# Kernel tuning notes

Hardware: AMD Instinct MI355X
Metric: run time of the kernel (lower is better)

Reference implementation:

```python
import jax, jax.numpy as jnp
import numpy as np

B, N, D, H = 4, 512, 4, 256


def _linear_params(key, fan_in, fan_out):
    # torch.nn.Linear default init: U(-1/sqrt(fan_in), 1/sqrt(fan_in))
    lim = 1.0 / np.sqrt(fan_in)
    kw, kb = jax.random.split(key)
    W = jax.random.uniform(kw, (fan_in, fan_out), minval=-lim, maxval=lim, dtype=jnp.float32)
    b = jax.random.uniform(kb, (fan_out,), minval=-lim, maxval=lim, dtype=jnp.float32)
    return W, b


def setup_inputs() -> dict:
    key = jax.random.key(0)
    ks = jax.random.split(key, 8)
    x = jax.random.normal(ks[0], (B, N, D), dtype=jnp.float32)
    adj = jax.random.uniform(ks[1], (B, N, N), dtype=jnp.float32)  # soft adjacency in [0,1)
    W_e1, b_e1 = _linear_params(ks[2], 2 * D, H)
    W_e2, b_e2 = _linear_params(ks[3], H, H)
    W_n1, b_n1 = _linear_params(ks[4], H, H)
    W_n2, b_n2 = _linear_params(ks[5], H, H)
    W_o1, b_o1 = _linear_params(ks[6], D + H, H)
    W_o, b_o = _linear_params(ks[7], H, D)
    return {
        "x": x, "adj": adj,
        "W_e1": W_e1, "b_e1": b_e1, "W_e2": W_e2, "b_e2": b_e2,
        "W_n1": W_n1, "b_n1": b_n1, "W_n2": W_n2, "b_n2": b_n2,
        "W_o1": W_o1, "b_o1": b_o1, "W_o": W_o, "b_o": b_o,
    }


def reference(x, adj, W_e1, b_e1, W_e2, b_e2, W_n1, b_n1, W_n2, b_n2, W_o1, b_o1, W_o, b_o):
    b_, n_, d_ = x.shape
    # innode[b,i,j,:] = x[b,j]; outnode[b,i,j,:] = x[b,i]
    innode = jnp.broadcast_to(x[:, None, :, :], (b_, n_, n_, d_))
    outnode = jnp.broadcast_to(x[:, :, None, :], (b_, n_, n_, d_))
    edge_in = jnp.concatenate([innode, outnode], axis=-1)          # [B,N,N,2D]
    node2edge = jax.nn.relu(edge_in @ W_e1 + b_e1)                 # [B,N,N,H]
    edge2edge = jax.nn.relu(node2edge @ W_e2 + b_e2)               # [B,N,N,H]
    # adjacency-masked sum over axis 1 (the i axis)
    agg = jnp.einsum('bij,bijh->bjh', adj, edge2edge)              # [B,N,H]
    out1 = jax.nn.relu(agg @ W_n1 + b_n1)
    out2 = jax.nn.relu(out1 @ W_n2 + b_n2)
    out3 = jnp.concatenate([x, out2], axis=-1)                     # [B,N,D+H]
    out4 = out3 @ W_o1 + b_o1
    out5 = out4 @ W_o + b_o                                        # [B,N,D]
    # CONTINUOUS is False for the classifier variant
    return jax.nn.log_softmax(out5, axis=2)
```

## Files before the change

kernel.cpp:

```cpp
#include <hip/hip_runtime.h>
#include <hip/hip_fp16.h>
#include <math.h>

#define Bq 4
#define Nq 512
#define Dq 4
#define Hq 256

typedef _Float16 f16x8 __attribute__((ext_vector_type(8)));
typedef float f32x4 __attribute__((ext_vector_type(4)));

__device__ __forceinline__ f16x8 hadd_relu(f16x8 u, f16x8 v) {
    f16x8 s = u + v;
    const f16x8 z = (f16x8)(_Float16)0.0f;
    return __builtin_elementwise_max(s, z);
}

__device__ __forceinline__ uint4 cvt8h(const float* p) {
    union { __half h[8]; uint4 u; } r;
#pragma unroll
    for (int i = 0; i < 8; ++i) r.h[i] = __float2half(p[i]);
    return r.u;
}

__global__ __launch_bounds__(256) void prep_all(
    const float* __restrict__ x, const float* __restrict__ We1,
    const float* __restrict__ be1, __half* __restrict__ U, __half* __restrict__ V,
    const float* __restrict__ Wn1, const float* __restrict__ Wn2,
    const float* __restrict__ Wo1, __half* __restrict__ Wt16) {
    const int bid = blockIdx.x;
    const int t = threadIdx.x;
    if (bid < 256) {
        const float w0 = We1[0 * 256 + t], w1 = We1[1 * 256 + t];
        const float w2 = We1[2 * 256 + t], w3 = We1[3 * 256 + t];
        const float w4 = We1[4 * 256 + t], w5 = We1[5 * 256 + t];
        const float w6 = We1[6 * 256 + t], w7 = We1[7 * 256 + t];
        const float bv = be1[t];
#pragma unroll
        for (int r = 0; r < 8; ++r) {
            const int row = bid * 8 + r;
            const float* xp = x + row * Dq;
            const float x0 = xp[0], x1 = xp[1], x2 = xp[2], x3 = xp[3];
            float u = bv;
            u = fmaf(x0, w0, u); u = fmaf(x1, w1, u);
            u = fmaf(x2, w2, u); u = fmaf(x3, w3, u);
            float v = x0 * w4;
            v = fmaf(x1, w5, v); v = fmaf(x2, w6, v); v = fmaf(x3, w7, v);
            U[(size_t)row * Hq + t] = __float2half(u);
            V[(size_t)row * Hq + t] = __float2half(v);
        }
    } else {
        __shared__ float ld[64][65];
        const int tid = bid - 256;
        const int mat = tid >> 4;
        const int tile = tid & 15;
        const int k0 = (tile >> 2) * 64;
        const int n0 = (tile & 3) * 64;
        const float* W = (mat == 0) ? Wn1 : (mat == 1) ? Wn2 : (Wo1 + 4 * 256);
        const int rr = t >> 6;
        const int cc = t & 63;
#pragma unroll
        for (int r = 0; r < 16; ++r) {
            const int row = r * 4 + rr;
            ld[row][cc] = W[(size_t)(k0 + row) * 256 + n0 + cc];
        }
        __syncthreads();
#pragma unroll
        for (int r = 0; r < 16; ++r) {
            const int nrow = r * 4 + rr;
            Wt16[((size_t)mat * 256 + n0 + nrow) * 256 + k0 + cc] =
                __float2half(ld[cc][nrow]);
        }
    }
}

__global__ __launch_bounds__(256, 2) void edge_gemm(
    const __half* __restrict__ U, const __half* __restrict__ V,
    const float* __restrict__ We2, const float* __restrict__ be2,
    const float* __restrict__ adj, float* __restrict__ aggws) {
    __shared__ __align__(16) char smem[59392];
    __half* Wt = (__half*)smem;
    __half* Us = (__half*)(smem + 32768);
    __half* Vs = (__half*)(smem + 40960);
    float* adjs = (float*)(smem + 57344);
    float* red = (float*)(smem + 40960);

    const int bid = blockIdx.x;
    const int hq_ = bid & 3;
    const int jt = (bid >> 2) & 31;
    const int b = bid >> 7;
    const int h_base = hq_ * 64;
    const int j_base = jt * 16;
    const int t = threadIdx.x;
    const int lane = t & 63;
    const int w = t >> 6;
    const int q = lane >> 4;
    const int l15 = lane & 15;

    const __half* Vb = V + (size_t)b * Nq * Hq;
    const float* adjb = adj + (size_t)b * Nq * Nq;

    const int srow = t >> 4;
    const int sc0 = (t & 15) * 2;

    {
        const int n = t & 63;
        const int swz = n & 31;
        for (int kk = (t >> 6); kk < 256; kk += 4) {
            float val = We2[kk * 256 + h_base + n];
            Wt[n * 256 + ((((kk >> 3) ^ swz)) << 3) + (kk & 7)] = __float2half(val);
        }
    }
    {
        const uint4* gp = (const uint4*)(U + (size_t)(b * Nq + j_base + srow) * Hq);
        uint4 v0 = gp[sc0];
        uint4 v1 = gp[sc0 + 1];
        *(uint4*)&Us[srow * 256 + ((sc0 ^ srow) << 3)] = v0;
        *(uint4*)&Us[srow * 256 + (((sc0 + 1) ^ srow) << 3)] = v1;
    }

    float bias[4];
#pragma unroll
    for (int nt = 0; nt < 4; ++nt) bias[nt] = be2[h_base + nt * 16 + l15];

    f32x4 agg[4];
#pragma unroll
    for (int nt = 0; nt < 4; ++nt) agg[nt] = (f32x4){0.f, 0.f, 0.f, 0.f};

    uint4 pva, pvb; float pad_;
    {
        const uint4* gp = (const uint4*)(Vb + (size_t)(0 + srow) * Hq);
        pva = gp[sc0]; pvb = gp[sc0 + 1];
        pad_ = adjb[(size_t)(0 + srow) * Nq + j_base + (t & 15)];
        *(uint4*)&Vs[0 * 4096 + srow * 256 + ((sc0 ^ srow) << 3)] = pva;
        *(uint4*)&Vs[0 * 4096 + srow * 256 + (((sc0 + 1) ^ srow) << 3)] = pvb;
        adjs[0 * 256 + t] = pad_;
    }
    {
        const uint4* gp = (const uint4*)(Vb + (size_t)(16 + srow) * Hq);
        pva = gp[sc0]; pvb = gp[sc0 + 1];
        pad_ = adjb[(size_t)(16 + srow) * Nq + j_base + (t & 15)];
    }
    __syncthreads();

    const f32x4 zero4 = (f32x4){0.f, 0.f, 0.f, 0.f};

    for (int ch = 0; ch < 32; ++ch) {
        const int cur = ch & 1;
        const __half* Vcur = Vs + cur * 4096;
        const float* Acur = adjs + cur * 256;

        f32x4 acc[4][4];
#pragma unroll
        for (int mi = 0; mi < 4; ++mi)
#pragma unroll
            for (int nt = 0; nt < 4; ++nt)
                acc[mi][nt] = (f32x4){bias[nt], bias[nt], bias[nt], bias[nt]};

#pragma unroll
        for (int ks = 0; ks < 8; ++ks) {
            const int c = ks * 4 + q;
            const f16x8 uvec = *(const f16x8*)&Us[l15 * 256 + ((c ^ l15) << 3)];
            f16x8 afrag[4];
#pragma unroll
            for (int mi = 0; mi < 4; ++mi) {
                const int iv = w * 4 + mi;
                const f16x8 vvec = *(const f16x8*)&Vcur[iv * 256 + ((c ^ iv) << 3)];
                afrag[mi] = hadd_relu(uvec, vvec);
            }
            f16x8 bf[4];
#pragma unroll
            for (int nt = 0; nt < 4; ++nt) {
                const int rn = nt * 16 + l15;
                bf[nt] = *(const f16x8*)&Wt[rn * 256 + ((c ^ (rn & 31)) << 3)];
            }
#pragma unroll
            for (int mi = 0; mi < 4; ++mi)
#pragma unroll
                for (int nt = 0; nt < 4; ++nt)
                    acc[mi][nt] = __builtin_amdgcn_mfma_f32_16x16x32_f16(
                        afrag[mi], bf[nt], acc[mi][nt], 0, 0, 0);
        }

#pragma unroll
        for (int mi = 0; mi < 4; ++mi) {
            const int iv = w * 4 + mi;
            const f32x4 av = *(const f32x4*)&Acur[iv * 16 + q * 4];
#pragma unroll
            for (int nt = 0; nt < 4; ++nt) {
                const f32x4 rel = __builtin_elementwise_max(acc[mi][nt], zero4);
                agg[nt] = av * rel + agg[nt];
            }
        }

        if (ch < 31) {
            const int nxt = cur ^ 1;
            *(uint4*)&Vs[nxt * 4096 + srow * 256 + ((sc0 ^ srow) << 3)] = pva;
            *(uint4*)&Vs[nxt * 4096 + srow * 256 + (((sc0 + 1) ^ srow) << 3)] = pvb;
            adjs[nxt * 256 + t] = pad_;
            if (ch < 30) {
                const int i_base = (ch + 2) * 16;
                const uint4* gp = (const uint4*)(Vb + (size_t)(i_base + srow) * Hq);
                pva = gp[sc0]; pvb = gp[sc0 + 1];
                pad_ = adjb[(size_t)(i_base + srow) * Nq + j_base + (t & 15)];
            }
        }
        __syncthreads();
    }

#pragma unroll
    for (int nt = 0; nt < 4; ++nt)
#pragma unroll
        for (int r = 0; r < 4; ++r)
            red[w * 1024 + (q * 4 + r) * 64 + nt * 16 + l15] = agg[nt][r];
    __syncthreads();
    {
        const int j = t >> 4;
        const int h0 = (t & 15) * 4;
        f32x4 s = *(const f32x4*)&red[0 * 1024 + j * 64 + h0];
        s += *(const f32x4*)&red[1 * 1024 + j * 64 + h0];
        s += *(const f32x4*)&red[2 * 1024 + j * 64 + h0];
        s += *(const f32x4*)&red[3 * 1024 + j * 64 + h0];
        *(f32x4*)&aggws[(size_t)(b * Nq + j_base + j) * Hq + h_base + h0] = s;
    }
}

__global__ __launch_bounds__(256) void tail_kernel(
    const float* __restrict__ aggws, const float* __restrict__ x,
    const __half* __restrict__ Wt16,
    const float* __restrict__ bn1, const float* __restrict__ bn2,
    const float* __restrict__ Wo1, const float* __restrict__ bo1,
    const float* __restrict__ Wo, const float* __restrict__ bo,
    float* __restrict__ out) {
    __shared__ __align__(16) __half actA[16 * 256];
    __shared__ __align__(16) __half actB[16 * 256];
    __shared__ float xs[16][4];
    __shared__ float part[4][16][4];
    __shared__ float s5[16][4];
    const int g0 = blockIdx.x * 16;
    const int t = threadIdx.x;
    const int lane = t & 63;
    const int w = t >> 6;
    const int q = lane >> 4;
    const int l15 = lane & 15;
    const int hb = w * 64;

    {
        const int row = t >> 4;
        const int g = (t & 15) * 2;
        const float* src = aggws + (size_t)(g0 + row) * 256;
        *(uint4*)&actA[row * 256 + ((g ^ row) << 3)] = cvt8h(src + g * 8);
        *(uint4*)&actA[row * 256 + (((g + 1) ^ row) << 3)] = cvt8h(src + g * 8 + 8);
    }
    if (t < 64) xs[t >> 2][t & 3] = x[(size_t)(g0 + (t >> 2)) * 4 + (t & 3)];
    __syncthreads();

    f32x4 acc[4];
#pragma unroll
    for (int nt = 0; nt < 4; ++nt) {
        const float bv = bn1[hb + nt * 16 + l15];
        acc[nt] = (f32x4){bv, bv, bv, bv};
    }
#pragma unroll
    for (int ks = 0; ks < 8; ++ks) {
        const int c = ks * 4 + q;
        const f16x8 af = *(const f16x8*)&actA[l15 * 256 + ((c ^ l15) << 3)];
#pragma unroll
        for (int nt = 0; nt < 4; ++nt) {
            const f16x8 bf = *(const f16x8*)&Wt16[(size_t)(hb + nt * 16 + l15) * 256 + c * 8];
            acc[nt] = __builtin_amdgcn_mfma_f32_16x16x32_f16(af, bf, acc[nt], 0, 0, 0);
        }
    }
#pragma unroll
    for (int nt = 0; nt < 4; ++nt) {
        const int n = hb + nt * 16 + l15;
        const int g = n >> 3;
#pragma unroll
        for (int r = 0; r < 4; ++r) {
            const int row = q * 4 + r;
            actB[row * 256 + ((g ^ row) << 3) + (n & 7)] = __float2half(fmaxf(acc[nt][r], 0.f));
        }
    }
    __syncthreads();

#pragma unroll
    for (int nt = 0; nt < 4; ++nt) {
        const float bv = bn2[hb + nt * 16 + l15];
        acc[nt] = (f32x4){bv, bv, bv, bv};
    }
#pragma unroll
    for (int ks = 0; ks < 8; ++ks) {
        const int c = ks * 4 + q;
        const f16x8 af = *(const f16x8*)&actB[l15 * 256 + ((c ^ l15) << 3)];
#pragma unroll
        for (int nt = 0; nt < 4; ++nt) {
            const f16x8 bf = *(const f16x8*)&Wt16[65536 + (size_t)(hb + nt * 16 + l15) * 256 + c * 8];
            acc[nt] = __builtin_amdgcn_mfma_f32_16x16x32_f16(af, bf, acc[nt], 0, 0, 0);
        }
    }
#pragma unroll
    for (int nt = 0; nt < 4; ++nt) {
        const int n = hb + nt * 16 + l15;
        const int g = n >> 3;
#pragma unroll
        for (int r = 0; r < 4; ++r) {
            const int row = q * 4 + r;
            actA[row * 256 + ((g ^ row) << 3) + (n & 7)] = __float2half(fmaxf(acc[nt][r], 0.f));
        }
    }
    __syncthreads();

#pragma unroll
    for (int nt = 0; nt < 4; ++nt) {
        const int n = hb + nt * 16 + l15;
        const float bv = bo1[n];
        const float w0 = Wo1[0 * 256 + n], w1 = Wo1[1 * 256 + n];
        const float w2 = Wo1[2 * 256 + n], w3 = Wo1[3 * 256 + n];
#pragma unroll
        for (int r = 0; r < 4; ++r) {
            const int row = q * 4 + r;
            float v = bv;
            v = fmaf(xs[row][0], w0, v); v = fmaf(xs[row][1], w1, v);
            v = fmaf(xs[row][2], w2, v); v = fmaf(xs[row][3], w3, v);
            acc[nt][r] = v;
        }
    }
#pragma unroll
    for (int ks = 0; ks < 8; ++ks) {
        const int c = ks * 4 + q;
        const f16x8 af = *(const f16x8*)&actA[l15 * 256 + ((c ^ l15) << 3)];
#pragma unroll
        for (int nt = 0; nt < 4; ++nt) {
            const f16x8 bf = *(const f16x8*)&Wt16[2 * 65536 + (size_t)(hb + nt * 16 + l15) * 256 + c * 8];
            acc[nt] = __builtin_amdgcn_mfma_f32_16x16x32_f16(af, bf, acc[nt], 0, 0, 0);
        }
    }

    float p[4][4];
#pragma unroll
    for (int r = 0; r < 4; ++r)
#pragma unroll
        for (int d = 0; d < 4; ++d) p[r][d] = 0.f;
#pragma unroll
    for (int nt = 0; nt < 4; ++nt) {
        const int n = hb + nt * 16 + l15;
        const float4 wv = *(const float4*)&Wo[n * 4];
#pragma unroll
        for (int r = 0; r < 4; ++r) {
            p[r][0] = fmaf(acc[nt][r], wv.x, p[r][0]);
            p[r][1] = fmaf(acc[nt][r], wv.y, p[r][1]);
            p[r][2] = fmaf(acc[nt][r], wv.z, p[r][2]);
            p[r][3] = fmaf(acc[nt][r], wv.w, p[r][3]);
        }
    }
#pragma unroll
    for (int off = 1; off < 16; off <<= 1)
#pragma unroll
        for (int r = 0; r < 4; ++r)
#pragma unroll
            for (int d = 0; d < 4; ++d)
                p[r][d] += __shfl_xor(p[r][d], off);
    if (l15 == 0) {
#pragma unroll
        for (int r = 0; r < 4; ++r)
#pragma unroll
            for (int d = 0; d < 4; ++d) part[w][q * 4 + r][d] = p[r][d];
    }
    __syncthreads();
    if (t < 64) {
        const int row = t >> 2;
        const int d = t & 3;
        s5[row][d] = part[0][row][d] + part[1][row][d] + part[2][row][d]
                   + part[3][row][d] + bo[d];
    }
    __syncthreads();
    if (t < 16) {
        const float v0 = s5[t][0], v1 = s5[t][1], v2 = s5[t][2], v3 = s5[t][3];
        const float m = fmaxf(fmaxf(v0, v1), fmaxf(v2, v3));
        const float s = expf(v0 - m) + expf(v1 - m) + expf(v2 - m) + expf(v3 - m);
        const float lse = m + logf(s);
        float* op = out + (size_t)(g0 + t) * 4;
        op[0] = v0 - lse; op[1] = v1 - lse; op[2] = v2 - lse; op[3] = v3 - lse;
    }
}

extern "C" void kernel_launch(void* const* d_in, const int* in_sizes, int n_in,
                              void* d_out, int out_size, void* d_ws, size_t ws_size,
                              hipStream_t stream) {
    const float* x   = (const float*)d_in[0];
    const float* adj = (const float*)d_in[1];
    const float* We1 = (const float*)d_in[2];
    const float* be1 = (const float*)d_in[3];
    const float* We2 = (const float*)d_in[4];
    const float* be2 = (const float*)d_in[5];
    const float* Wn1 = (const float*)d_in[6];
    const float* bn1 = (const float*)d_in[7];
    const float* Wn2 = (const float*)d_in[8];
    const float* bn2 = (const float*)d_in[9];
    const float* Wo1 = (const float*)d_in[10];
    const float* bo1 = (const float*)d_in[11];
    const float* Wo  = (const float*)d_in[12];
    const float* bo  = (const float*)d_in[13];
    float* out = (float*)d_out;

    __half* U = (__half*)d_ws;
    __half* V = U + (size_t)Bq * Nq * Hq;
    float* aggws = (float*)((char*)d_ws + (size_t)2 * Bq * Nq * Hq * sizeof(__half));
    __half* Wt16 = (__half*)((char*)d_ws + (size_t)4 * 1024 * 1024);

    prep_all<<<304, 256, 0, stream>>>(x, We1, be1, U, V, Wn1, Wn2, Wo1, Wt16);
    edge_gemm<<<512, 256, 0, stream>>>(U, V, We2, be2, adj, aggws);
    tail_kernel<<<128, 256, 0, stream>>>(aggws, x, Wt16, bn1, bn2, Wo1, bo1, Wo, bo, out);
}
```

Baseline: 227.3 us.

## Double edge_gemm block to 512 threads with 32-row i chunks

```diff
diff --git a/kernel.cpp b/kernel.cpp
--- a/kernel.cpp
+++ b/kernel.cpp
@@ -74,15 +74,15 @@
     }
 }
 
-__global__ __launch_bounds__(256, 2) void edge_gemm(
+__global__ __launch_bounds__(512, 4) void edge_gemm(
     const __half* __restrict__ U, const __half* __restrict__ V,
     const float* __restrict__ We2, const float* __restrict__ be2,
     const float* __restrict__ adj, float* __restrict__ aggws) {
-    __shared__ __align__(16) char smem[59392];
+    __shared__ __align__(16) char smem[77824];
     __half* Wt = (__half*)smem;
     __half* Us = (__half*)(smem + 32768);
     __half* Vs = (__half*)(smem + 40960);
-    float* adjs = (float*)(smem + 57344);
+    float* adjs = (float*)(smem + 73728);
     float* red = (float*)(smem + 40960);
 
     const int bid = blockIdx.x;
@@ -106,17 +106,19 @@
     {
         const int n = t & 63;
         const int swz = n & 31;
-        for (int kk = (t >> 6); kk < 256; kk += 4) {
+        for (int kk = (t >> 6); kk < 256; kk += 8) {
             float val = We2[kk * 256 + h_base + n];
             Wt[n * 256 + ((((kk >> 3) ^ swz)) << 3) + (kk & 7)] = __float2half(val);
         }
     }
-    {
-        const uint4* gp = (const uint4*)(U + (size_t)(b * Nq + j_base + srow) * Hq);
-        uint4 v0 = gp[sc0];
-        uint4 v1 = gp[sc0 + 1];
-        *(uint4*)&Us[srow * 256 + ((sc0 ^ srow) << 3)] = v0;
-        *(uint4*)&Us[srow * 256 + (((sc0 + 1) ^ srow) << 3)] = v1;
+    if (t < 256) {
+        const int sr = t >> 4;
+        const int g0 = (t & 15) * 2;
+        const uint4* gp = (const uint4*)(U + (size_t)(b * Nq + j_base + sr) * Hq);
+        uint4 v0 = gp[g0];
+        uint4 v1 = gp[g0 + 1];
+        *(uint4*)&Us[sr * 256 + ((g0 ^ sr) << 3)] = v0;
+        *(uint4*)&Us[sr * 256 + (((g0 + 1) ^ sr) << 3)] = v1;
     }
 
     float bias[4];
@@ -129,26 +131,26 @@
 
     uint4 pva, pvb; float pad_;
     {
-        const uint4* gp = (const uint4*)(Vb + (size_t)(0 + srow) * Hq);
+        const uint4* gp = (const uint4*)(Vb + (size_t)srow * Hq);
         pva = gp[sc0]; pvb = gp[sc0 + 1];
-        pad_ = adjb[(size_t)(0 + srow) * Nq + j_base + (t & 15)];
-        *(uint4*)&Vs[0 * 4096 + srow * 256 + ((sc0 ^ srow) << 3)] = pva;
-        *(uint4*)&Vs[0 * 4096 + srow * 256 + (((sc0 + 1) ^ srow) << 3)] = pvb;
-        adjs[0 * 256 + t] = pad_;
+        pad_ = adjb[(size_t)srow * Nq + j_base + (t & 15)];
+        *(uint4*)&Vs[srow * 256 + ((sc0 ^ srow) << 3)] = pva;
+        *(uint4*)&Vs[srow * 256 + (((sc0 + 1) ^ srow) << 3)] = pvb;
+        adjs[t] = pad_;
     }
     {
-        const uint4* gp = (const uint4*)(Vb + (size_t)(16 + srow) * Hq);
+        const uint4* gp = (const uint4*)(Vb + (size_t)(32 + srow) * Hq);
         pva = gp[sc0]; pvb = gp[sc0 + 1];
-        pad_ = adjb[(size_t)(16 + srow) * Nq + j_base + (t & 15)];
+        pad_ = adjb[(size_t)(32 + srow) * Nq + j_base + (t & 15)];
     }
     __syncthreads();
 
     const f32x4 zero4 = (f32x4){0.f, 0.f, 0.f, 0.f};
 
-    for (int ch = 0; ch < 32; ++ch) {
+    for (int ch = 0; ch < 16; ++ch) {
         const int cur = ch & 1;
-        const __half* Vcur = Vs + cur * 4096;
-        const float* Acur = adjs + cur * 256;
+        const __half* Vcur = Vs + cur * 8192;
+        const float* Acur = adjs + cur * 512;
 
         f32x4 acc[4][4];
 #pragma unroll
@@ -193,13 +195,13 @@
             }
         }
 
-        if (ch < 31) {
+        if (ch < 15) {
             const int nxt = cur ^ 1;
-            *(uint4*)&Vs[nxt * 4096 + srow * 256 + ((sc0 ^ srow) << 3)] = pva;
-            *(uint4*)&Vs[nxt * 4096 + srow * 256 + (((sc0 + 1) ^ srow) << 3)] = pvb;
-            adjs[nxt * 256 + t] = pad_;
-            if (ch < 30) {
-                const int i_base = (ch + 2) * 16;
+            *(uint4*)&Vs[nxt * 8192 + srow * 256 + ((sc0 ^ srow) << 3)] = pva;
+            *(uint4*)&Vs[nxt * 8192 + srow * 256 + (((sc0 + 1) ^ srow) << 3)] = pvb;
+            adjs[nxt * 512 + t] = pad_;
+            if (ch < 14) {
+                const int i_base = (ch + 2) * 32;
                 const uint4* gp = (const uint4*)(Vb + (size_t)(i_base + srow) * Hq);
                 pva = gp[sc0]; pvb = gp[sc0 + 1];
                 pad_ = adjb[(size_t)(i_base + srow) * Nq + j_base + (t & 15)];
@@ -214,13 +216,13 @@
         for (int r = 0; r < 4; ++r)
             red[w * 1024 + (q * 4 + r) * 64 + nt * 16 + l15] = agg[nt][r];
     __syncthreads();
-    {
+    if (t < 256) {
         const int j = t >> 4;
         const int h0 = (t & 15) * 4;
         f32x4 s = *(const f32x4*)&red[0 * 1024 + j * 64 + h0];
-        s += *(const f32x4*)&red[1 * 1024 + j * 64 + h0];
-        s += *(const f32x4*)&red[2 * 1024 + j * 64 + h0];
-        s += *(const f32x4*)&red[3 * 1024 + j * 64 + h0];
+#pragma unroll
+        for (int ww = 1; ww < 8; ++ww)
+            s += *(const f32x4*)&red[ww * 1024 + j * 64 + h0];
         *(f32x4*)&aggws[(size_t)(b * Nq + j_base + j) * Hq + h_base + h0] = s;
     }
 }
@@ -409,6 +411,6 @@
     __half* Wt16 = (__half*)((char*)d_ws + (size_t)4 * 1024 * 1024);
 
     prep_all<<<304, 256, 0, stream>>>(x, We1, be1, U, V, Wn1, Wn2, Wo1, Wt16);
-    edge_gemm<<<512, 256, 0, stream>>>(U, V, We2, be2, adj, aggws);
+    edge_gemm<<<512, 512, 0, stream>>>(U, V, We2, be2, adj, aggws);
     tail_kernel<<<128, 256, 0, stream>>>(aggws, x, Wt16, bn1, bn2, Wo1, bo1, Wo, bo, out);
 }
```

Measured after the change: 464.4 us. 104% more time.

## Split edge GEMM over i halves with atomic reduction and global pre-transposed We2

Applied to the files above, without the earlier changes.

```diff
diff --git a/kernel.cpp b/kernel.cpp
--- a/kernel.cpp
+++ b/kernel.cpp
@@ -27,10 +27,17 @@
     const float* __restrict__ x, const float* __restrict__ We1,
     const float* __restrict__ be1, __half* __restrict__ U, __half* __restrict__ V,
     const float* __restrict__ Wn1, const float* __restrict__ Wn2,
-    const float* __restrict__ Wo1, __half* __restrict__ Wt16) {
+    const float* __restrict__ Wo1, const float* __restrict__ We2,
+    __half* __restrict__ Wt16, float* __restrict__ aggz) {
     const int bid = blockIdx.x;
     const int t = threadIdx.x;
     if (bid < 256) {
+        {
+            float* az = aggz + (size_t)bid * 2048 + t * 8;
+            const f32x4 z4 = (f32x4){0.f, 0.f, 0.f, 0.f};
+            *(f32x4*)az = z4;
+            *(f32x4*)(az + 4) = z4;
+        }
         const float w0 = We1[0 * 256 + t], w1 = We1[1 * 256 + t];
         const float w2 = We1[2 * 256 + t], w3 = We1[3 * 256 + t];
         const float w4 = We1[4 * 256 + t], w5 = We1[5 * 256 + t];
@@ -56,7 +63,8 @@
         const int tile = tid & 15;
         const int k0 = (tile >> 2) * 64;
         const int n0 = (tile & 3) * 64;
-        const float* W = (mat == 0) ? Wn1 : (mat == 1) ? Wn2 : (Wo1 + 4 * 256);
+        const float* W = (mat == 0) ? Wn1 : (mat == 1) ? Wn2
+                       : (mat == 2) ? (Wo1 + 4 * 256) : We2;
         const int rr = t >> 6;
         const int cc = t & 63;
 #pragma unroll
@@ -74,23 +82,24 @@
     }
 }
 
-__global__ __launch_bounds__(256, 2) void edge_gemm(
+__global__ __launch_bounds__(256, 4) void edge_gemm(
     const __half* __restrict__ U, const __half* __restrict__ V,
-    const float* __restrict__ We2, const float* __restrict__ be2,
+    const __half* __restrict__ We2t, const float* __restrict__ be2,
     const float* __restrict__ adj, float* __restrict__ aggws) {
-    __shared__ __align__(16) char smem[59392];
-    __half* Wt = (__half*)smem;
-    __half* Us = (__half*)(smem + 32768);
-    __half* Vs = (__half*)(smem + 40960);
-    float* adjs = (float*)(smem + 57344);
-    float* red = (float*)(smem + 40960);
+    __shared__ __align__(16) char smem[26624];
+    __half* Us = (__half*)smem;
+    __half* Vs = (__half*)(smem + 8192);
+    float* adjs = (float*)(smem + 24576);
+    float* red = (float*)(smem + 8192);
 
     const int bid = blockIdx.x;
-    const int hq_ = bid & 3;
-    const int jt = (bid >> 2) & 31;
-    const int b = bid >> 7;
+    const int jt = bid & 31;
+    const int ih = (bid >> 5) & 1;
+    const int hq_ = (bid >> 6) & 3;
+    const int b = bid >> 8;
     const int h_base = hq_ * 64;
     const int j_base = jt * 16;
+    const int i0 = ih * 256;
     const int t = threadIdx.x;
     const int lane = t & 63;
     const int w = t >> 6;
@@ -103,14 +112,6 @@
     const int srow = t >> 4;
     const int sc0 = (t & 15) * 2;
 
-    {
-        const int n = t & 63;
-        const int swz = n & 31;
-        for (int kk = (t >> 6); kk < 256; kk += 4) {
-            float val = We2[kk * 256 + h_base + n];
-            Wt[n * 256 + ((((kk >> 3) ^ swz)) << 3) + (kk & 7)] = __float2half(val);
-        }
-    }
     {
         const uint4* gp = (const uint4*)(U + (size_t)(b * Nq + j_base + srow) * Hq);
         uint4 v0 = gp[sc0];
@@ -129,26 +130,31 @@
 
     uint4 pva, pvb; float pad_;
     {
-        const uint4* gp = (const uint4*)(Vb + (size_t)(0 + srow) * Hq);
+        const uint4* gp = (const uint4*)(Vb + (size_t)(i0 + srow) * Hq);
         pva = gp[sc0]; pvb = gp[sc0 + 1];
-        pad_ = adjb[(size_t)(0 + srow) * Nq + j_base + (t & 15)];
-        *(uint4*)&Vs[0 * 4096 + srow * 256 + ((sc0 ^ srow) << 3)] = pva;
-        *(uint4*)&Vs[0 * 4096 + srow * 256 + (((sc0 + 1) ^ srow) << 3)] = pvb;
-        adjs[0 * 256 + t] = pad_;
+        pad_ = adjb[(size_t)(i0 + srow) * Nq + j_base + (t & 15)];
+        *(uint4*)&Vs[srow * 256 + ((sc0 ^ srow) << 3)] = pva;
+        *(uint4*)&Vs[srow * 256 + (((sc0 + 1) ^ srow) << 3)] = pvb;
+        adjs[t] = pad_;
     }
     {
-        const uint4* gp = (const uint4*)(Vb + (size_t)(16 + srow) * Hq);
+        const uint4* gp = (const uint4*)(Vb + (size_t)(i0 + 16 + srow) * Hq);
         pva = gp[sc0]; pvb = gp[sc0 + 1];
-        pad_ = adjb[(size_t)(16 + srow) * Nq + j_base + (t & 15)];
+        pad_ = adjb[(size_t)(i0 + 16 + srow) * Nq + j_base + (t & 15)];
     }
     __syncthreads();
 
     const f32x4 zero4 = (f32x4){0.f, 0.f, 0.f, 0.f};
-
-    for (int ch = 0; ch < 32; ++ch) {
+    const __half* WrowBase = We2t + (size_t)(h_base + l15) * 256 + q * 8;
+
+    for (int ch = 0; ch < 16; ++ch) {
         const int cur = ch & 1;
         const __half* Vcur = Vs + cur * 4096;
         const float* Acur = adjs + cur * 256;
+
+        int zofs = 0;
+        asm volatile("" : "+v"(zofs));
+        const __half* Wrow = WrowBase + zofs;
 
         f32x4 acc[4][4];
 #pragma unroll
@@ -170,10 +176,8 @@
             }
             f16x8 bf[4];
 #pragma unroll
-            for (int nt = 0; nt < 4; ++nt) {
-                const int rn = nt * 16 + l15;
-                bf[nt] = *(const f16x8*)&Wt[rn * 256 + ((c ^ (rn & 31)) << 3)];
-            }
+            for (int nt = 0; nt < 4; ++nt)
+                bf[nt] = *(const f16x8*)&Wrow[nt * 4096 + ks * 32];
 #pragma unroll
             for (int mi = 0; mi < 4; ++mi)
 #pragma unroll
@@ -193,13 +197,13 @@
             }
         }
 
-        if (ch < 31) {
+        if (ch < 15) {
             const int nxt = cur ^ 1;
             *(uint4*)&Vs[nxt * 4096 + srow * 256 + ((sc0 ^ srow) << 3)] = pva;
             *(uint4*)&Vs[nxt * 4096 + srow * 256 + (((sc0 + 1) ^ srow) << 3)] = pvb;
             adjs[nxt * 256 + t] = pad_;
-            if (ch < 30) {
-                const int i_base = (ch + 2) * 16;
+            if (ch < 14) {
+                const int i_base = i0 + (ch + 2) * 16;
                 const uint4* gp = (const uint4*)(Vb + (size_t)(i_base + srow) * Hq);
                 pva = gp[sc0]; pvb = gp[sc0 + 1];
                 pad_ = adjb[(size_t)(i_base + srow) * Nq + j_base + (t & 15)];
@@ -221,7 +225,11 @@
         s += *(const f32x4*)&red[1 * 1024 + j * 64 + h0];
         s += *(const f32x4*)&red[2 * 1024 + j * 64 + h0];
         s += *(const f32x4*)&red[3 * 1024 + j * 64 + h0];
-        *(f32x4*)&aggws[(size_t)(b * Nq + j_base + j) * Hq + h_base + h0] = s;
+        float* dst = &aggws[(size_t)(b * Nq + j_base + j) * Hq + h_base + h0];
+        atomicAdd(dst + 0, s[0]);
+        atomicAdd(dst + 1, s[1]);
+        atomicAdd(dst + 2, s[2]);
+        atomicAdd(dst + 3, s[3]);
     }
 }
 
@@ -407,8 +415,9 @@
     __half* V = U + (size_t)Bq * Nq * Hq;
     float* aggws = (float*)((char*)d_ws + (size_t)2 * Bq * Nq * Hq * sizeof(__half));
     __half* Wt16 = (__half*)((char*)d_ws + (size_t)4 * 1024 * 1024);
-
-    prep_all<<<304, 256, 0, stream>>>(x, We1, be1, U, V, Wn1, Wn2, Wo1, Wt16);
-    edge_gemm<<<512, 256, 0, stream>>>(U, V, We2, be2, adj, aggws);
+    __half* We2t = Wt16 + (size_t)3 * 65536;
+
+    prep_all<<<320, 256, 0, stream>>>(x, We1, be1, U, V, Wn1, Wn2, Wo1, We2, Wt16, aggws);
+    edge_gemm<<<1024, 256, 0, stream>>>(U, V, We2t, be2, adj, aggws);
     tail_kernel<<<128, 256, 0, stream>>>(aggws, x, Wt16, bn1, bn2, Wo1, bo1, Wo, bo, out);
 }
```

Measured after the change: 506.4 us. 123% more time.

## Split edge_gemm across 8 waves, each covering half the hidden columns

Applied to the files above, without the earlier changes.

```diff
diff --git a/kernel.cpp b/kernel.cpp
--- a/kernel.cpp
+++ b/kernel.cpp
@@ -74,7 +74,7 @@
     }
 }
 
-__global__ __launch_bounds__(256, 2) void edge_gemm(
+__global__ __launch_bounds__(512, 2) void edge_gemm(
     const __half* __restrict__ U, const __half* __restrict__ V,
     const float* __restrict__ We2, const float* __restrict__ be2,
     const float* __restrict__ adj, float* __restrict__ aggws) {
@@ -94,52 +94,52 @@
     const int t = threadIdx.x;
     const int lane = t & 63;
     const int w = t >> 6;
+    const int wi = w & 3;
+    const int wh = w >> 2;
     const int q = lane >> 4;
     const int l15 = lane & 15;
 
     const __half* Vb = V + (size_t)b * Nq * Hq;
     const float* adjb = adj + (size_t)b * Nq * Nq;
 
-    const int srow = t >> 4;
-    const int sc0 = (t & 15) * 2;
+    const int sr5 = t >> 5;
+    const int g5 = t & 31;
 
     {
         const int n = t & 63;
         const int swz = n & 31;
-        for (int kk = (t >> 6); kk < 256; kk += 4) {
+        for (int kk = (t >> 6); kk < 256; kk += 8) {
             float val = We2[kk * 256 + h_base + n];
             Wt[n * 256 + ((((kk >> 3) ^ swz)) << 3) + (kk & 7)] = __float2half(val);
         }
     }
     {
-        const uint4* gp = (const uint4*)(U + (size_t)(b * Nq + j_base + srow) * Hq);
-        uint4 v0 = gp[sc0];
-        uint4 v1 = gp[sc0 + 1];
-        *(uint4*)&Us[srow * 256 + ((sc0 ^ srow) << 3)] = v0;
-        *(uint4*)&Us[srow * 256 + (((sc0 + 1) ^ srow) << 3)] = v1;
-    }
-
-    float bias[4];
-#pragma unroll
-    for (int nt = 0; nt < 4; ++nt) bias[nt] = be2[h_base + nt * 16 + l15];
-
-    f32x4 agg[4];
-#pragma unroll
-    for (int nt = 0; nt < 4; ++nt) agg[nt] = (f32x4){0.f, 0.f, 0.f, 0.f};
-
-    uint4 pva, pvb; float pad_;
+        const uint4* gp = (const uint4*)(U + (size_t)(b * Nq + j_base + sr5) * Hq);
+        *(uint4*)&Us[sr5 * 256 + ((g5 ^ sr5) << 3)] = gp[g5];
+    }
+
+    float bias[2];
+#pragma unroll
+    for (int nt = 0; nt < 2; ++nt) bias[nt] = be2[h_base + wh * 32 + nt * 16 + l15];
+
+    f32x4 agg[2];
+#pragma unroll
+    for (int nt = 0; nt < 2; ++nt) agg[nt] = (f32x4){0.f, 0.f, 0.f, 0.f};
+
+    uint4 pva; float pad_;
     {
-        const uint4* gp = (const uint4*)(Vb + (size_t)(0 + srow) * Hq);
-        pva = gp[sc0]; pvb = gp[sc0 + 1];
-        pad_ = adjb[(size_t)(0 + srow) * Nq + j_base + (t & 15)];
-        *(uint4*)&Vs[0 * 4096 + srow * 256 + ((sc0 ^ srow) << 3)] = pva;
-        *(uint4*)&Vs[0 * 4096 + srow * 256 + (((sc0 + 1) ^ srow) << 3)] = pvb;
-        adjs[0 * 256 + t] = pad_;
+        const uint4* gp = (const uint4*)(Vb + (size_t)sr5 * Hq);
+        pva = gp[g5];
+        *(uint4*)&Vs[sr5 * 256 + g5 * 8] = pva;
+        if (t < 256) {
+            pad_ = adjb[(size_t)(t >> 4) * Nq + j_base + (t & 15)];
+            adjs[t] = pad_;
+        }
     }
     {
-        const uint4* gp = (const uint4*)(Vb + (size_t)(16 + srow) * Hq);
-        pva = gp[sc0]; pvb = gp[sc0 + 1];
-        pad_ = adjb[(size_t)(16 + srow) * Nq + j_base + (t & 15)];
+        const uint4* gp = (const uint4*)(Vb + (size_t)(16 + sr5) * Hq);
+        pva = gp[g5];
+        if (t < 256) pad_ = adjb[(size_t)(16 + (t >> 4)) * Nq + j_base + (t & 15)];
     }
     __syncthreads();
 
@@ -150,11 +150,11 @@
         const __half* Vcur = Vs + cur * 4096;
         const float* Acur = adjs + cur * 256;
 
-        f32x4 acc[4][4];
+        f32x4 acc[4][2];
 #pragma unroll
         for (int mi = 0; mi < 4; ++mi)
 #pragma unroll
-            for (int nt = 0; nt < 4; ++nt)
+            for (int nt = 0; nt < 2; ++nt)
                 acc[mi][nt] = (f32x4){bias[nt], bias[nt], bias[nt], bias[nt]};
 
 #pragma unroll
@@ -164,30 +164,30 @@
             f16x8 afrag[4];
 #pragma unroll
             for (int mi = 0; mi < 4; ++mi) {
-                const int iv = w * 4 + mi;
-                const f16x8 vvec = *(const f16x8*)&Vcur[iv * 256 + ((c ^ iv) << 3)];
+                const int iv = wi * 4 + mi;
+                const f16x8 vvec = *(const f16x8*)&Vcur[iv * 256 + c * 8];
                 afrag[mi] = hadd_relu(uvec, vvec);
             }
-            f16x8 bf[4];
-#pragma unroll
-            for (int nt = 0; nt < 4; ++nt) {
-                const int rn = nt * 16 + l15;
+            f16x8 bf[2];
+#pragma unroll
+            for (int nt = 0; nt < 2; ++nt) {
+                const int rn = wh * 32 + nt * 16 + l15;
                 bf[nt] = *(const f16x8*)&Wt[rn * 256 + ((c ^ (rn & 31)) << 3)];
             }
 #pragma unroll
             for (int mi = 0; mi < 4; ++mi)
 #pragma unroll
-                for (int nt = 0; nt < 4; ++nt)
+                for (int nt = 0; nt < 2; ++nt)
                     acc[mi][nt] = __builtin_amdgcn_mfma_f32_16x16x32_f16(
                         afrag[mi], bf[nt], acc[mi][nt], 0, 0, 0);
         }
 
 #pragma unroll
         for (int mi = 0; mi < 4; ++mi) {
-            const int iv = w * 4 + mi;
+            const int iv = wi * 4 + mi;
             const f32x4 av = *(const f32x4*)&Acur[iv * 16 + q * 4];
 #pragma unroll
-            for (int nt = 0; nt < 4; ++nt) {
+            for (int nt = 0; nt < 2; ++nt) {
                 const f32x4 rel = __builtin_elementwise_max(acc[mi][nt], zero4);
                 agg[nt] = av * rel + agg[nt];
             }
@@ -195,33 +195,36 @@
 
         if (ch < 31) {
             const int nxt = cur ^ 1;
-            *(uint4*)&Vs[nxt * 4096 + srow * 256 + ((sc0 ^ srow) << 3)] = pva;
-            *(uint4*)&Vs[nxt * 4096 + srow * 256 + (((sc0 + 1) ^ srow) << 3)] = pvb;
-            adjs[nxt * 256 + t] = pad_;
+            *(uint4*)&Vs[nxt * 4096 + sr5 * 256 + g5 * 8] = pva;
+            if (t < 256) adjs[nxt * 256 + t] = pad_;
             if (ch < 30) {
                 const int i_base = (ch + 2) * 16;
-                const uint4* gp = (const uint4*)(Vb + (size_t)(i_base + srow) * Hq);
-                pva = gp[sc0]; pvb = gp[sc0 + 1];
-                pad_ = adjb[(size_t)(i_base + srow) * Nq + j_base + (t & 15)];
+                const uint4* gp = (const uint4*)(Vb + (size_t)(i_base + sr5) * Hq);
+                pva = gp[g5];
+                if (t < 256)
+                    pad_ = adjb[(size_t)(i_base + (t >> 4)) * Nq + j_base + (t & 15)];
             }
         }
         __syncthreads();
     }
 
 #pragma unroll
-    for (int nt = 0; nt < 4; ++nt)
+    for (int nt = 0; nt < 2; ++nt)
 #pragma unroll
         for (int r = 0; r < 4; ++r)
-            red[w * 1024 + (q * 4 + r) * 64 + nt * 16 + l15] = agg[nt][r];
-    __syncthreads();
-    {
+            red[wh * 2048 + wi * 512 + (q * 4 + r) * 32 + nt * 16 + l15] = agg[nt][r];
+    __syncthreads();
+    if (t < 256) {
         const int j = t >> 4;
-        const int h0 = (t & 15) * 4;
-        f32x4 s = *(const f32x4*)&red[0 * 1024 + j * 64 + h0];
-        s += *(const f32x4*)&red[1 * 1024 + j * 64 + h0];
-        s += *(const f32x4*)&red[2 * 1024 + j * 64 + h0];
-        s += *(const f32x4*)&red[3 * 1024 + j * 64 + h0];
-        *(f32x4*)&aggws[(size_t)(b * Nq + j_base + j) * Hq + h_base + h0] = s;
+        const int h16 = t & 15;
+        const int wh2 = h16 >> 3;
+        const int hc = (h16 & 7) * 4;
+        const int base = wh2 * 2048 + j * 32 + hc;
+        f32x4 s = *(const f32x4*)&red[base];
+        s += *(const f32x4*)&red[base + 512];
+        s += *(const f32x4*)&red[base + 1024];
+        s += *(const f32x4*)&red[base + 1536];
+        *(f32x4*)&aggws[(size_t)(b * Nq + j_base + j) * Hq + h_base + h16 * 4] = s;
     }
 }
 
@@ -409,6 +412,6 @@
     __half* Wt16 = (__half*)((char*)d_ws + (size_t)4 * 1024 * 1024);
 
     prep_all<<<304, 256, 0, stream>>>(x, We1, be1, U, V, Wn1, Wn2, Wo1, Wt16);
-    edge_gemm<<<512, 256, 0, stream>>>(U, V, We2, be2, adj, aggws);
+    edge_gemm<<<512, 512, 0, stream>>>(U, V, We2, be2, adj, aggws);
     tail_kernel<<<128, 256, 0, stream>>>(aggws, x, Wt16, bn1, bn2, Wo1, bo1, Wo, bo, out);
 }
```

Result: slower. 255.7 us (+12.5%).
